# Kernel optimization log

Hardware: AMD Instinct MI355X
Metric: run time of the kernel (lower is better)

The kernel has to match this reference:

```python
import jax, jax.numpy as jnp
import numpy as np

BIG = 3.4028234e+38  # torch fill value used as additive mask
EPS = 1e-5           # nn.LayerNorm default eps


def _layernorm(x):
    mu = jnp.mean(x, axis=-1, keepdims=True)
    var = jnp.mean(jnp.square(x - mu), axis=-1, keepdims=True)
    return (x - mu) / jnp.sqrt(var + EPS)


def setup_inputs() -> dict:
    key = jax.random.key(0)
    ks = jax.random.split(key, 12)
    B, N, H, S = 32, 512, 256, 3  # batch, num_codes, embedding_size, num_stacks
    features = jax.random.normal(ks[0], (B, N, H), dtype=jnp.float32)
    masks = jnp.ones((B, N, 1), dtype=jnp.float32)
    guide = jax.random.randint(ks[1], (B, N, N), 0, 2).astype(jnp.float32)
    prior_guide = jax.random.uniform(ks[2], (B, N, N), dtype=jnp.float32)
    sc = 0.02
    WQ = jax.random.normal(ks[3], (S, H, H), dtype=jnp.float32) * sc
    WK = jax.random.normal(ks[4], (S, H, H), dtype=jnp.float32) * sc
    WV = jax.random.normal(ks[5], (S, H, H), dtype=jnp.float32) * sc
    W1 = jax.random.normal(ks[6], (S, H, H), dtype=jnp.float32) * sc
    b1 = jnp.zeros((S, H), dtype=jnp.float32)
    W2 = jax.random.normal(ks[7], (S, H, H), dtype=jnp.float32) * sc
    b2 = jnp.zeros((S, H), dtype=jnp.float32)
    return {"features": features, "masks": masks, "guide": guide,
            "prior_guide": prior_guide, "WQ": WQ, "WK": WK, "WV": WV,
            "W1": W1, "b1": b1, "W2": W2, "b2": b2}


def reference(features, masks, guide, prior_guide, WQ, WK, WV, W1, b1, W2, b2):
    H = features.shape[-1]
    scale = 1.0 / jnp.sqrt(jnp.float32(H))
    attention_mask = jnp.where(masks[:, :, 0] != 0, 0.0, BIG)  # [B,N]
    inf_mask = jnp.where(guide != 0, 0.0, BIG)                 # [B,N,N]
    attentions = []
    x = features
    for i in range(WQ.shape[0]):
        f = masks * x                                          # [B,N,H]
        if i == 0:
            att = prior_guide[:, None, :, :]                   # use_prior path
        else:
            q = jnp.einsum('bnh,hd->bnd', f, WQ[i].T)          # nn.Linear: x @ W^T
            k = jnp.einsum('bnh,hd->bnd', f, WK[i].T)
            pre = jnp.einsum('bqd,bkd->bqk', q, k) * scale     # [B,N,N] (heads=1)
            pre = pre - attention_mask[:, None, :] - inf_mask
            att = jax.nn.softmax(pre, axis=-1)[:, None, :, :]  # [B,1,N,N]
        attentions.append(att)
        v = jnp.einsum('bnh,hd->bnd', f, WV[i].T)              # [B,N,H]
        post = jnp.einsum('bqk,bkh->bqh', att[:, 0], v)        # squeeze head dim
        post = _layernorm(post + f)
        ffn = jnp.maximum(jnp.einsum('bnh,hd->bnd', post, W1[i].T) + b1[i], 0.0)
        ffn = jnp.einsum('bnh,hd->bnd', ffn, W2[i].T) + b2[i]
        x = _layernorm(ffn + post)
    return x * masks, jnp.stack(attentions)
```

## Files before the change

kernel.cpp:

```cpp
#include <hip/hip_runtime.h>
#include <cstdint>
#include <cstddef>

#define B_ 32
#define N_ 512
#define H_ 256
#define S_ 3
#define BN_ (B_*N_)
#define HH_ (H_*H_)
#define BIGF 3.4028234e+38f
#define EPSF 1e-5f
#define SF_ ((long)N_ * H_)
#define SVT_ ((long)H_ * N_)

typedef __bf16 bf16x8 __attribute__((ext_vector_type(8)));
typedef float  f32x4  __attribute__((ext_vector_type(4)));

typedef const void __attribute__((address_space(1)))* gas_t;
typedef void __attribute__((address_space(3)))* las_t;

__device__ __forceinline__ void async16(const unsigned short* g, unsigned short* l) {
  __builtin_amdgcn_global_load_lds((gas_t)g, (las_t)l, 16, 0, 0);
}

__device__ __forceinline__ unsigned short f2bf(float f) {
  __bf16 h = (__bf16)f;
  unsigned short s;
  __builtin_memcpy(&s, &h, 2);
  return s;
}
__device__ __forceinline__ float bf2f(unsigned short u) {
  unsigned int v = ((unsigned int)u) << 16;
  float f;
  __builtin_memcpy(&f, &v, 4);
  return f;
}

#define KC_STAGE(lane) ((((lane) & 3) ^ (((lane) >> 3) & 3)) * 8)
#define KC_READ(quad, l15) ((((quad) ^ (((l15) >> 1) & 3))) * 8)

__global__ __launch_bounds__(256) void cvt_all_k(
    const float* __restrict__ WQ, const float* __restrict__ WK,
    const float* __restrict__ WV, const float* __restrict__ W1,
    const float* __restrict__ W2,
    unsigned short* __restrict__ wqk, unsigned short* __restrict__ wv,
    unsigned short* __restrict__ w1, unsigned short* __restrict__ w2) {
  const int per = S_ * HH_ / 4;
  int gi = blockIdx.x * 256 + threadIdx.x;
  int which = gi / per;
  int e4 = gi - which * per;
  float4 v;
  if      (which == 0) v = ((const float4*)WQ)[e4];
  else if (which == 1) v = ((const float4*)WK)[e4];
  else if (which == 2) v = ((const float4*)WV)[e4];
  else if (which == 3) v = ((const float4*)W1)[e4];
  else                 v = ((const float4*)W2)[e4];
  ushort4 o;
  o.x = f2bf(v.x); o.y = f2bf(v.y); o.z = f2bf(v.z); o.w = f2bf(v.w);
  int e = e4 * 4;
  if (which <= 1) {
    int L = e / HH_, off = e - L * HH_;
    *(ushort4*)&wqk[(size_t)L * 2 * HH_ + (which == 1 ? HH_ : 0) + off] = o;
  } else if (which == 2) ((ushort4*)wv)[e4] = o;
  else if   (which == 3) ((ushort4*)w1)[e4] = o;
  else                   ((ushort4*)w2)[e4] = o;
}

__global__ __launch_bounds__(256) void mask_mul_k(
    const float* __restrict__ x, const float* __restrict__ masks,
    unsigned short* __restrict__ fb) {
  int i = blockIdx.x * 256 + threadIdx.x;
  int row = i >> 6;
  float m = masks[row];
  float4 v = ((const float4*)x)[i];
  ushort4 o;
  o.x = f2bf(v.x * m); o.y = f2bf(v.y * m); o.z = f2bf(v.z * m); o.w = f2bf(v.w * m);
  ((ushort4*)fb)[i] = o;
}

__device__ __forceinline__ void gemm_body(
    const unsigned short* __restrict__ A, const unsigned short* __restrict__ Bm,
    unsigned short* __restrict__ Cb,
    int K, int Nn, int lda, int ldb, long sA, long sB, long sC,
    int b, int m0, int n0, int t,
    unsigned short (&As)[2][128 * 32], unsigned short (&Bs)[2][128 * 32]) {
  const int wave = t >> 6, lane = t & 63;
  const int wm = wave >> 1, wn = wave & 1;
  const int quad = lane >> 4, l15 = lane & 15;
  const int srow = lane >> 2;
  const int kc = KC_STAGE(lane);
  const int pos8 = (lane & 3) * 8;

  const unsigned short* pa0 = A + (size_t)b * sA + (size_t)(m0 + wave * 32 + srow) * lda + kc;
  const unsigned short* pa1 = pa0 + 16 * (size_t)lda;
  const unsigned short* pb0 = Bm + (size_t)b * sB + (size_t)(n0 + wave * 32 + srow) * ldb + kc;
  const unsigned short* pb1 = pb0 + 16 * (size_t)ldb;
  const int lo = (wave * 32 + srow) * 32 + pos8;

  f32x4 acc[4][4];
#pragma unroll
  for (int i = 0; i < 4; ++i)
#pragma unroll
    for (int j = 0; j < 4; ++j) acc[i][j] = (f32x4){0.f, 0.f, 0.f, 0.f};

  const int soff = KC_READ(quad, l15);
  const int NT = K >> 5;
  async16(pa0, &As[0][lo]); async16(pa1, &As[0][lo + 16 * 32]);
  async16(pb0, &Bs[0][lo]); async16(pb1, &Bs[0][lo + 16 * 32]);
  __syncthreads();
  int cur = 0;
  for (int tt = 0; tt < NT; ++tt) {
    if (tt + 1 < NT) {
      const int kn = (tt + 1) << 5;
      async16(pa0 + kn, &As[cur ^ 1][lo]); async16(pa1 + kn, &As[cur ^ 1][lo + 16 * 32]);
      async16(pb0 + kn, &Bs[cur ^ 1][lo]); async16(pb1 + kn, &Bs[cur ^ 1][lo + 16 * 32]);
    }
    bf16x8 af[4], bfr[4];
#pragma unroll
    for (int i = 0; i < 4; ++i)
      af[i] = *(const bf16x8*)&As[cur][(wm * 64 + i * 16 + l15) * 32 + soff];
#pragma unroll
    for (int j = 0; j < 4; ++j)
      bfr[j] = *(const bf16x8*)&Bs[cur][(wn * 64 + j * 16 + l15) * 32 + soff];
#pragma unroll
    for (int i = 0; i < 4; ++i)
#pragma unroll
      for (int j = 0; j < 4; ++j)
        acc[i][j] = __builtin_amdgcn_mfma_f32_16x16x32_bf16(af[i], bfr[j], acc[i][j], 0, 0, 0);
    __syncthreads();
    cur ^= 1;
  }

#pragma unroll
  for (int i = 0; i < 4; ++i) {
    const int rbase = m0 + wm * 64 + i * 16 + quad * 4;
#pragma unroll
    for (int j = 0; j < 4; ++j) {
      const int c = n0 + wn * 64 + j * 16 + l15;
#pragma unroll
      for (int r = 0; r < 4; ++r)
        Cb[(size_t)b * sC + (size_t)(rbase + r) * Nn + c] = f2bf(acc[i][j][r]);
    }
  }
}

__global__ __launch_bounds__(256) void mfma_gemm_k(
    const unsigned short* __restrict__ A, const unsigned short* __restrict__ Bm,
    unsigned short* __restrict__ Cb,
    int K, int Nn, int lda, int ldb, long sA, long sB, long sC) {
  __shared__ __align__(16) unsigned short As[2][128 * 32];
  __shared__ __align__(16) unsigned short Bs[2][128 * 32];
  gemm_body(A, Bm, Cb, K, Nn, lda, ldb, sA, sB, sC,
            blockIdx.z, blockIdx.y * 128, blockIdx.x * 128, threadIdx.x, As, Bs);
}

__global__ __launch_bounds__(256) void gemm2_k(
    const unsigned short* __restrict__ A1, const unsigned short* __restrict__ B1,
    unsigned short* __restrict__ C1,
    const unsigned short* __restrict__ A2, const unsigned short* __restrict__ B2,
    unsigned short* __restrict__ C2) {
  __shared__ __align__(16) unsigned short As[2][128 * 32];
  __shared__ __align__(16) unsigned short Bs[2][128 * 32];
  const int bx = blockIdx.x;
  if (bx < 512) {
    gemm_body(A1, B1, C1, H_, 2 * H_, H_, H_, 0, 0, 0,
              0, (bx >> 2) * 128, (bx & 3) * 128, threadIdx.x, As, Bs);
  } else {
    const int v = bx - 512;
    gemm_body(A2, B2, C2, H_, N_, H_, H_, 0, SF_, SVT_,
              v >> 3, ((v >> 2) & 1) * 128, (v & 3) * 128, threadIdx.x, As, Bs);
  }
}

template<int PRIOR, int LAST>
__global__ __launch_bounds__(512) void mega_k(
    const unsigned short* __restrict__ qk, const float* __restrict__ prior,
    const float* __restrict__ masks, const float* __restrict__ guide,
    const unsigned short* __restrict__ vT, const unsigned short* __restrict__ resb,
    const unsigned short* __restrict__ w1, const float* __restrict__ b1,
    const unsigned short* __restrict__ w2, const float* __restrict__ b2,
    float* __restrict__ att, unsigned short* __restrict__ fbout,
    float* __restrict__ outx) {
  __shared__ __align__(16) unsigned short As[2][64 * 32];
  __shared__ __align__(16) unsigned short Bs[2][512 * 32];
  __shared__ __align__(16) unsigned short PsU[64 * 528];
  __shared__ float red[4][64][2];
  const int b = blockIdx.x;
  const int t = threadIdx.x;
  const int wave = t >> 6, lane = t & 63;
  const int quad = lane >> 4, l15 = lane & 15;
  const int m0 = blockIdx.y * 64;
  const int srow = lane >> 2;
  const int kc = KC_STAGE(lane);
  const int pos8 = (lane & 3) * 8;
  const int soff = KC_READ(quad, l15);

  const unsigned short* vb = vT + (size_t)b * SVT_;
  const unsigned short* pv0 = vb + (size_t)(wave * 16 + srow) * N_ + kc;
  const unsigned short* pv1 = pv0 + (size_t)128 * N_;
  const int lvo = (wave * 16 + srow) * 32 + pos8;

  if (PRIOR) {
    async16(pv0, &Bs[0][lvo]);
    async16(pv1, &Bs[0][lvo + 128 * 32]);
    const float* src = prior + ((size_t)b * N_ + m0) * N_;
    float*       dst = att   + ((size_t)b * N_ + m0) * N_;
#pragma unroll
    for (int s = 0; s < 16; ++s) {
      int idx4 = s * 512 + t;
      float4 v = ((const float4*)src)[idx4];
      ((float4*)dst)[idx4] = v;
      int row = idx4 >> 7, col4 = idx4 & 127;
      ushort4 o;
      o.x = f2bf(v.x); o.y = f2bf(v.y); o.z = f2bf(v.z); o.w = f2bf(v.w);
      *(ushort4*)&PsU[row * 520 + col4 * 4] = o;
    }
    __syncthreads();
  } else {
    const int wm = wave >> 2, wn = wave & 3;
    const int ld = 2 * H_;
    const unsigned short* base = qk + (size_t)b * N_ * ld;
    const unsigned short* pa = base + (size_t)(m0 + wave * 16 + srow) * ld + kc;
    const unsigned short* pb = base + H_ + (size_t)(wave * 64 + srow) * ld + kc;
    const int lao = (wave * 16 + srow) * 32 + pos8;
    const int lbo = (wave * 64 + srow) * 32 + pos8;

    f32x4 acc[2][8];
#pragma unroll
    for (int i = 0; i < 2; ++i)
#pragma unroll
      for (int j = 0; j < 8; ++j) acc[i][j] = (f32x4){0.f, 0.f, 0.f, 0.f};

    if (wave < 4) async16(pa, &As[0][lao]);
#pragma unroll
    for (int c = 0; c < 4; ++c)
      async16(pb + (size_t)c * 16 * ld, &Bs[0][lbo + c * 16 * 32]);
    __syncthreads();
    int cur = 0;
#pragma unroll
    for (int tt = 0; tt < 8; ++tt) {
      if (tt < 7) {
        const int kn = (tt + 1) * 32;
        if (wave < 4) async16(pa + kn, &As[cur ^ 1][lao]);
#pragma unroll
        for (int c = 0; c < 4; ++c)
          async16(pb + (size_t)c * 16 * ld + kn, &Bs[cur ^ 1][lbo + c * 16 * 32]);
      }
      bf16x8 af[2], bfr[8];
#pragma unroll
      for (int i = 0; i < 2; ++i)
        af[i] = *(const bf16x8*)&As[cur][(wm * 32 + i * 16 + l15) * 32 + soff];
#pragma unroll
      for (int j = 0; j < 8; ++j)
        bfr[j] = *(const bf16x8*)&Bs[cur][(wn * 128 + j * 16 + l15) * 32 + soff];
#pragma unroll
      for (int i = 0; i < 2; ++i)
#pragma unroll
        for (int j = 0; j < 8; ++j)
          acc[i][j] = __builtin_amdgcn_mfma_f32_16x16x32_bf16(af[i], bfr[j], acc[i][j], 0, 0, 0);
      __syncthreads();
      cur ^= 1;
    }

    async16(pv0, &Bs[0][lvo]);
    async16(pv1, &Bs[0][lvo + 128 * 32]);

    float am[8];
#pragma unroll
    for (int j = 0; j < 8; ++j) {
      float mv = masks[(size_t)b * N_ + wn * 128 + j * 16 + l15];
      am[j] = (mv != 0.f) ? 0.f : BIGF;
    }
#pragma unroll
    for (int i = 0; i < 2; ++i) {
#pragma unroll
      for (int r = 0; r < 4; ++r) {
        const int mloc = wm * 32 + i * 16 + quad * 4 + r;
        const float* gr = guide + ((size_t)b * N_ + m0 + mloc) * N_;
        float mx = -BIGF;
#pragma unroll
        for (int j = 0; j < 8; ++j) {
          const int c = wn * 128 + j * 16 + l15;
          float g = gr[c];
          float v = acc[i][j][r] * 0.0625f - am[j] - ((g != 0.f) ? 0.f : BIGF);
          acc[i][j][r] = v;
          mx = fmaxf(mx, v);
        }
#pragma unroll
        for (int off = 1; off < 16; off <<= 1) mx = fmaxf(mx, __shfl_xor(mx, off));
        if (l15 == 0) red[wn][mloc][0] = mx;
      }
    }
    __syncthreads();
#pragma unroll
    for (int i = 0; i < 2; ++i) {
#pragma unroll
      for (int r = 0; r < 4; ++r) {
        const int mloc = wm * 32 + i * 16 + quad * 4 + r;
        float M = fmaxf(fmaxf(red[0][mloc][0], red[1][mloc][0]),
                        fmaxf(red[2][mloc][0], red[3][mloc][0]));
        float s = 0.f;
#pragma unroll
        for (int j = 0; j < 8; ++j) {
          float e = __expf(acc[i][j][r] - M);
          acc[i][j][r] = e;
          s += e;
        }
#pragma unroll
        for (int off = 1; off < 16; off <<= 1) s += __shfl_xor(s, off);
        if (l15 == 0) red[wn][mloc][1] = s;
      }
    }
    __syncthreads();
#pragma unroll
    for (int i = 0; i < 2; ++i) {
#pragma unroll
      for (int r = 0; r < 4; ++r) {
        const int mloc = wm * 32 + i * 16 + quad * 4 + r;
        float S = red[0][mloc][1] + red[1][mloc][1] + red[2][mloc][1] + red[3][mloc][1];
        float inv = 1.f / S;
        const size_t rowoff = ((size_t)b * N_ + m0 + mloc) * N_;
#pragma unroll
        for (int j = 0; j < 8; ++j) {
          const int c = wn * 128 + j * 16 + l15;
          float o = acc[i][j][r] * inv;
          att[rowoff + c] = o;
          PsU[mloc * 520 + c] = f2bf(o);
        }
      }
    }
    __syncthreads();
  }

  const int wm2 = wave >> 2, wn2 = wave & 3;

  f32x4 acc2[2][4];
#pragma unroll
  for (int i = 0; i < 2; ++i)
#pragma unroll
    for (int j = 0; j < 4; ++j) acc2[i][j] = (f32x4){0.f, 0.f, 0.f, 0.f};

  int cur = 0;
#pragma unroll
  for (int tt = 0; tt < 16; ++tt) {
    if (tt < 15) {
      const int kn = (tt + 1) * 32;
      async16(pv0 + kn, &Bs[cur ^ 1][lvo]);
      async16(pv1 + kn, &Bs[cur ^ 1][lvo + 128 * 32]);
    }
    bf16x8 af[2], bfr[4];
#pragma unroll
    for (int i = 0; i < 2; ++i)
      af[i] = *(const bf16x8*)&PsU[(wm2 * 32 + i * 16 + l15) * 520 + tt * 32 + quad * 8];
#pragma unroll
    for (int j = 0; j < 4; ++j)
      bfr[j] = *(const bf16x8*)&Bs[cur][(wn2 * 64 + j * 16 + l15) * 32 + soff];
#pragma unroll
    for (int i = 0; i < 2; ++i)
#pragma unroll
      for (int j = 0; j < 4; ++j)
        acc2[i][j] = __builtin_amdgcn_mfma_f32_16x16x32_bf16(af[i], bfr[j], acc2[i][j], 0, 0, 0);
    __syncthreads();
    cur ^= 1;
  }

  const unsigned short* pw1  = w1 + (size_t)(wave * 16 + srow) * H_ + kc;
  const unsigned short* pw1b = pw1 + (size_t)128 * H_;
  const unsigned short* pw2  = w2 + (size_t)(wave * 16 + srow) * H_ + kc;
  const unsigned short* pw2b = pw2 + (size_t)128 * H_;
  async16(pw1,  &Bs[0][lvo]);
  async16(pw1b, &Bs[0][lvo + 128 * 32]);

#pragma unroll
  for (int i = 0; i < 2; ++i) {
#pragma unroll
    for (int r = 0; r < 4; ++r) {
      const int mloc = wm2 * 32 + i * 16 + quad * 4 + r;
      const long grow = (long)b * N_ + m0 + mloc;
      float s = 0.f, q = 0.f;
#pragma unroll
      for (int j = 0; j < 4; ++j) {
        const int c = wn2 * 64 + j * 16 + l15;
        float v = acc2[i][j][r] + bf2f(resb[grow * H_ + c]);
        acc2[i][j][r] = v;
        s += v; q += v * v;
      }
#pragma unroll
      for (int off = 1; off < 16; off <<= 1) {
        s += __shfl_xor(s, off);
        q += __shfl_xor(q, off);
      }
      if (l15 == 0) { red[wn2][mloc][0] = s; red[wn2][mloc][1] = q; }
    }
  }
  __syncthreads();
  unsigned short* Pb  = PsU;
  unsigned short* T1p = PsU + 64 * 264;
#pragma unroll
  for (int i = 0; i < 2; ++i) {
#pragma unroll
    for (int r = 0; r < 4; ++r) {
      const int mloc = wm2 * 32 + i * 16 + quad * 4 + r;
      float S = red[0][mloc][0] + red[1][mloc][0] + red[2][mloc][0] + red[3][mloc][0];
      float Q = red[0][mloc][1] + red[1][mloc][1] + red[2][mloc][1] + red[3][mloc][1];
      float mu = S * (1.f / H_);
      float var = Q * (1.f / H_) - mu * mu;
      float inv = 1.f / sqrtf(var + EPSF);
#pragma unroll
      for (int j = 0; j < 4; ++j) {
        const int c = wn2 * 64 + j * 16 + l15;
        float o = (acc2[i][j][r] - mu) * inv;
        acc2[i][j][r] = o;
        Pb[mloc * 264 + c] = f2bf(o);
      }
    }
  }
  __syncthreads();

  {
    f32x4 acc3[2][4];
#pragma unroll
    for (int i = 0; i < 2; ++i)
#pragma unroll
      for (int j = 0; j < 4; ++j) acc3[i][j] = (f32x4){0.f, 0.f, 0.f, 0.f};
    cur = 0;
#pragma unroll
    for (int tt = 0; tt < 8; ++tt) {
      if (tt < 7) {
        const int kn = (tt + 1) * 32;
        async16(pw1  + kn, &Bs[cur ^ 1][lvo]);
        async16(pw1b + kn, &Bs[cur ^ 1][lvo + 128 * 32]);
      }
      bf16x8 af[2], bfr[4];
#pragma unroll
      for (int i = 0; i < 2; ++i)
        af[i] = *(const bf16x8*)&Pb[(wm2 * 32 + i * 16 + l15) * 264 + tt * 32 + quad * 8];
#pragma unroll
      for (int j = 0; j < 4; ++j)
        bfr[j] = *(const bf16x8*)&Bs[cur][(wn2 * 64 + j * 16 + l15) * 32 + soff];
#pragma unroll
      for (int i = 0; i < 2; ++i)
#pragma unroll
        for (int j = 0; j < 4; ++j)
          acc3[i][j] = __builtin_amdgcn_mfma_f32_16x16x32_bf16(af[i], bfr[j], acc3[i][j], 0, 0, 0);
      __syncthreads();
      cur ^= 1;
    }

    async16(pw2,  &Bs[0][lvo]);
    async16(pw2b, &Bs[0][lvo + 128 * 32]);

    float bv[4];
#pragma unroll
    for (int j = 0; j < 4; ++j) bv[j] = b1[wn2 * 64 + j * 16 + l15];
#pragma unroll
    for (int i = 0; i < 2; ++i) {
#pragma unroll
      for (int r = 0; r < 4; ++r) {
        const int mloc = wm2 * 32 + i * 16 + quad * 4 + r;
#pragma unroll
        for (int j = 0; j < 4; ++j) {
          const int c = wn2 * 64 + j * 16 + l15;
          T1p[mloc * 264 + c] = f2bf(fmaxf(acc3[i][j][r] + bv[j], 0.f));
        }
      }
    }
  }
  __syncthreads();

  {
    f32x4 acc4[2][4];
#pragma unroll
    for (int i = 0; i < 2; ++i)
#pragma unroll
      for (int j = 0; j < 4; ++j) acc4[i][j] = (f32x4){0.f, 0.f, 0.f, 0.f};
    cur = 0;
#pragma unroll
    for (int tt = 0; tt < 8; ++tt) {
      if (tt < 7) {
        const int kn = (tt + 1) * 32;
        async16(pw2  + kn, &Bs[cur ^ 1][lvo]);
        async16(pw2b + kn, &Bs[cur ^ 1][lvo + 128 * 32]);
      }
      bf16x8 af[2], bfr[4];
#pragma unroll
      for (int i = 0; i < 2; ++i)
        af[i] = *(const bf16x8*)&T1p[(wm2 * 32 + i * 16 + l15) * 264 + tt * 32 + quad * 8];
#pragma unroll
      for (int j = 0; j < 4; ++j)
        bfr[j] = *(const bf16x8*)&Bs[cur][(wn2 * 64 + j * 16 + l15) * 32 + soff];
#pragma unroll
      for (int i = 0; i < 2; ++i)
#pragma unroll
        for (int j = 0; j < 4; ++j)
          acc4[i][j] = __builtin_amdgcn_mfma_f32_16x16x32_bf16(af[i], bfr[j], acc4[i][j], 0, 0, 0);
      __syncthreads();
      cur ^= 1;
    }
    float bv[4];
#pragma unroll
    for (int j = 0; j < 4; ++j) bv[j] = b2[wn2 * 64 + j * 16 + l15];
#pragma unroll
    for (int i = 0; i < 2; ++i) {
#pragma unroll
      for (int r = 0; r < 4; ++r) {
        const int mloc = wm2 * 32 + i * 16 + quad * 4 + r;
        float s = 0.f, q = 0.f;
#pragma unroll
        for (int j = 0; j < 4; ++j) {
          float v = acc4[i][j][r] + bv[j] + acc2[i][j][r];
          acc4[i][j][r] = v;
          s += v; q += v * v;
        }
#pragma unroll
        for (int off = 1; off < 16; off <<= 1) {
          s += __shfl_xor(s, off);
          q += __shfl_xor(q, off);
        }
        if (l15 == 0) { red[wn2][mloc][0] = s; red[wn2][mloc][1] = q; }
      }
    }
    __syncthreads();
#pragma unroll
    for (int i = 0; i < 2; ++i) {
#pragma unroll
      for (int r = 0; r < 4; ++r) {
        const int mloc = wm2 * 32 + i * 16 + quad * 4 + r;
        const long grow = (long)b * N_ + m0 + mloc;
        float S = red[0][mloc][0] + red[1][mloc][0] + red[2][mloc][0] + red[3][mloc][0];
        float Q = red[0][mloc][1] + red[1][mloc][1] + red[2][mloc][1] + red[3][mloc][1];
        float mu = S * (1.f / H_);
        float var = Q * (1.f / H_) - mu * mu;
        float inv = 1.f / sqrtf(var + EPSF);
        float mval = masks[grow];
#pragma unroll
        for (int j = 0; j < 4; ++j) {
          const int c = wn2 * 64 + j * 16 + l15;
          float o = (acc4[i][j][r] - mu) * inv * mval;
          if (LAST) outx[grow * H_ + c] = o;
          else      fbout[grow * H_ + c] = f2bf(o);
        }
      }
    }
  }
}

extern "C" void kernel_launch(void* const* d_in, const int* in_sizes, int n_in,
                              void* d_out, int out_size, void* d_ws, size_t ws_size,
                              hipStream_t stream) {
  const float* features = (const float*)d_in[0];
  const float* masks    = (const float*)d_in[1];
  const float* guide    = (const float*)d_in[2];
  const float* prior    = (const float*)d_in[3];
  const float* WQ       = (const float*)d_in[4];
  const float* WK       = (const float*)d_in[5];
  const float* WV       = (const float*)d_in[6];
  const float* W1       = (const float*)d_in[7];
  const float* b1       = (const float*)d_in[8];
  const float* W2       = (const float*)d_in[9];
  const float* b2       = (const float*)d_in[10];

  float* out     = (float*)d_out;
  float* out_x   = out;
  float* out_att = out + (size_t)BN_ * H_;

  char* w = (char*)d_ws;
  unsigned short* f_bf   = (unsigned short*)w; w += (size_t)BN_ * H_ * 2;
  unsigned short* qk_bf  = (unsigned short*)w; w += (size_t)BN_ * 2 * H_ * 2;
  unsigned short* vT     = (unsigned short*)w; w += (size_t)BN_ * H_ * 2;
  unsigned short* wqk_bf = (unsigned short*)w; w += (size_t)S_ * 2 * HH_ * 2;
  unsigned short* wv_bf  = (unsigned short*)w; w += (size_t)S_ * HH_ * 2;
  unsigned short* w1_bf  = (unsigned short*)w; w += (size_t)S_ * HH_ * 2;
  unsigned short* w2_bf  = (unsigned short*)w; w += (size_t)S_ * HH_ * 2;

  dim3 g_cvt(5 * S_ * HH_ / 1024);
  dim3 g_ew(BN_ * H_ / 1024);
  dim3 g_vt(4, 2, B_);
  dim3 g_g2(768);
  dim3 g_mega(B_, N_ / 64);

  cvt_all_k<<<g_cvt, 256, 0, stream>>>(WQ, WK, WV, W1, W2, wqk_bf, wv_bf, w1_bf, w2_bf);
  mask_mul_k<<<g_ew, 256, 0, stream>>>(features, masks, f_bf);

  for (int i = 0; i < S_; ++i) {
    float* att = out_att + (size_t)i * B_ * N_ * N_;
    const unsigned short* w1p = w1_bf + (size_t)i * HH_;
    const unsigned short* w2p = w2_bf + (size_t)i * HH_;
    const float* b1p = b1 + (size_t)i * H_;
    const float* b2p = b2 + (size_t)i * H_;
    if (i == 0) {
      mfma_gemm_k<<<g_vt, 256, 0, stream>>>(wv_bf, f_bf, vT, H_, N_, H_, H_, 0, SF_, SVT_);
      mega_k<1, 0><<<g_mega, 512, 0, stream>>>(nullptr, prior, masks, nullptr,
                                               vT, f_bf, w1p, b1p, w2p, b2p,
                                               att, f_bf, nullptr);
    } else {
      gemm2_k<<<g_g2, 256, 0, stream>>>(f_bf, wqk_bf + (size_t)i * 2 * HH_, qk_bf,
                                        wv_bf + (size_t)i * HH_, f_bf, vT);
      if (i < S_ - 1) {
        mega_k<0, 0><<<g_mega, 512, 0, stream>>>(qk_bf, nullptr, masks, guide,
                                                 vT, f_bf, w1p, b1p, w2p, b2p,
                                                 att, f_bf, nullptr);
      } else {
        mega_k<0, 1><<<g_mega, 512, 0, stream>>>(qk_bf, nullptr, masks, guide,
                                                 vT, f_bf, w1p, b1p, w2p, b2p,
                                                 att, nullptr, out_x);
      }
    }
  }
}
```

Before: 339.3 us.

## Double mega kernel to 1024 threads, add nontemporal streams and finer GEMM sync

Launches the fused attention/FFN mega kernel with 16 waves instead of 8 and splits each GEMM stage's N dimension across 8 wave columns, so each wave holds fewer accumulators and issues fewer async loads. The large attention, prior and output streams switch to nontemporal loads and stores to avoid polluting cache. The generic GEMM body replaces __syncthreads with explicit vmcnt waits plus barriers so the next tile's prefetch stays in flight. The extra waves raise register and barrier pressure per block and give less MFMA work per wave.

Result: slower. 351.1 us (+3.5%).

```diff
diff --git a/kernel.cpp b/kernel.cpp
--- a/kernel.cpp
+++ b/kernel.cpp
@@ -22,6 +22,10 @@
 __device__ __forceinline__ void async16(const unsigned short* g, unsigned short* l) {
   __builtin_amdgcn_global_load_lds((gas_t)g, (las_t)l, 16, 0, 0);
 }
+
+#define VMW(n) asm volatile("s_waitcnt vmcnt(" #n ")" ::: "memory")
+#define SB()   __builtin_amdgcn_s_barrier()
+#define SC0()  __builtin_amdgcn_sched_barrier(0)
 
 __device__ __forceinline__ unsigned short f2bf(float f) {
   __bf16 h = (__bf16)f;
@@ -107,14 +111,15 @@
   const int NT = K >> 5;
   async16(pa0, &As[0][lo]); async16(pa1, &As[0][lo + 16 * 32]);
   async16(pb0, &Bs[0][lo]); async16(pb1, &Bs[0][lo + 16 * 32]);
-  __syncthreads();
   int cur = 0;
   for (int tt = 0; tt < NT; ++tt) {
     if (tt + 1 < NT) {
       const int kn = (tt + 1) << 5;
       async16(pa0 + kn, &As[cur ^ 1][lo]); async16(pa1 + kn, &As[cur ^ 1][lo + 16 * 32]);
       async16(pb0 + kn, &Bs[cur ^ 1][lo]); async16(pb1 + kn, &Bs[cur ^ 1][lo + 16 * 32]);
-    }
+      VMW(4);
+    } else VMW(0);
+    SB(); SC0();
     bf16x8 af[4], bfr[4];
 #pragma unroll
     for (int i = 0; i < 4; ++i)
@@ -127,7 +132,7 @@
 #pragma unroll
       for (int j = 0; j < 4; ++j)
         acc[i][j] = __builtin_amdgcn_mfma_f32_16x16x32_bf16(af[i], bfr[j], acc[i][j], 0, 0, 0);
-    __syncthreads();
+    SC0(); SB();
     cur ^= 1;
   }
 
@@ -173,7 +178,7 @@
 }
 
 template<int PRIOR, int LAST>
-__global__ __launch_bounds__(512) void mega_k(
+__global__ __launch_bounds__(1024) void mega_k(
     const unsigned short* __restrict__ qk, const float* __restrict__ prior,
     const float* __restrict__ masks, const float* __restrict__ guide,
     const unsigned short* __restrict__ vT, const unsigned short* __restrict__ resb,
@@ -184,7 +189,7 @@
   __shared__ __align__(16) unsigned short As[2][64 * 32];
   __shared__ __align__(16) unsigned short Bs[2][512 * 32];
   __shared__ __align__(16) unsigned short PsU[64 * 528];
-  __shared__ float red[4][64][2];
+  __shared__ float red[8][64][2];
   const int b = blockIdx.x;
   const int t = threadIdx.x;
   const int wave = t >> 6, lane = t & 63;
@@ -194,22 +199,20 @@
   const int kc = KC_STAGE(lane);
   const int pos8 = (lane & 3) * 8;
   const int soff = KC_READ(quad, l15);
-
-  const unsigned short* vb = vT + (size_t)b * SVT_;
-  const unsigned short* pv0 = vb + (size_t)(wave * 16 + srow) * N_ + kc;
-  const unsigned short* pv1 = pv0 + (size_t)128 * N_;
+  const int wm = wave >> 3, wn = wave & 7;
+
+  const unsigned short* pv = vT + (size_t)b * SVT_ + (size_t)(wave * 16 + srow) * N_ + kc;
   const int lvo = (wave * 16 + srow) * 32 + pos8;
 
   if (PRIOR) {
-    async16(pv0, &Bs[0][lvo]);
-    async16(pv1, &Bs[0][lvo + 128 * 32]);
-    const float* src = prior + ((size_t)b * N_ + m0) * N_;
-    float*       dst = att   + ((size_t)b * N_ + m0) * N_;
-#pragma unroll
-    for (int s = 0; s < 16; ++s) {
-      int idx4 = s * 512 + t;
-      float4 v = ((const float4*)src)[idx4];
-      ((float4*)dst)[idx4] = v;
+    async16(pv, &Bs[0][lvo]);
+    const f32x4* src = (const f32x4*)(prior + ((size_t)b * N_ + m0) * N_);
+    f32x4*       dst = (f32x4*)(att   + ((size_t)b * N_ + m0) * N_);
+#pragma unroll
+    for (int s = 0; s < 8; ++s) {
+      int idx4 = s * 1024 + t;
+      f32x4 v = __builtin_nontemporal_load(&src[idx4]);
+      __builtin_nontemporal_store(v, &dst[idx4]);
       int row = idx4 >> 7, col4 = idx4 & 127;
       ushort4 o;
       o.x = f2bf(v.x); o.y = f2bf(v.y); o.z = f2bf(v.z); o.w = f2bf(v.w);
@@ -217,23 +220,22 @@
     }
     __syncthreads();
   } else {
-    const int wm = wave >> 2, wn = wave & 3;
     const int ld = 2 * H_;
     const unsigned short* base = qk + (size_t)b * N_ * ld;
     const unsigned short* pa = base + (size_t)(m0 + wave * 16 + srow) * ld + kc;
-    const unsigned short* pb = base + H_ + (size_t)(wave * 64 + srow) * ld + kc;
+    const unsigned short* pb = base + H_ + (size_t)(wave * 32 + srow) * ld + kc;
     const int lao = (wave * 16 + srow) * 32 + pos8;
-    const int lbo = (wave * 64 + srow) * 32 + pos8;
-
-    f32x4 acc[2][8];
+    const int lbo = (wave * 32 + srow) * 32 + pos8;
+
+    f32x4 acc[2][4];
 #pragma unroll
     for (int i = 0; i < 2; ++i)
 #pragma unroll
-      for (int j = 0; j < 8; ++j) acc[i][j] = (f32x4){0.f, 0.f, 0.f, 0.f};
+      for (int j = 0; j < 4; ++j) acc[i][j] = (f32x4){0.f, 0.f, 0.f, 0.f};
 
     if (wave < 4) async16(pa, &As[0][lao]);
 #pragma unroll
-    for (int c = 0; c < 4; ++c)
+    for (int c = 0; c < 2; ++c)
       async16(pb + (size_t)c * 16 * ld, &Bs[0][lbo + c * 16 * 32]);
     __syncthreads();
     int cur = 0;
@@ -243,32 +245,31 @@
         const int kn = (tt + 1) * 32;
         if (wave < 4) async16(pa + kn, &As[cur ^ 1][lao]);
 #pragma unroll
-        for (int c = 0; c < 4; ++c)
+        for (int c = 0; c < 2; ++c)
           async16(pb + (size_t)c * 16 * ld + kn, &Bs[cur ^ 1][lbo + c * 16 * 32]);
       }
-      bf16x8 af[2], bfr[8];
+      bf16x8 af[2], bfr[4];
 #pragma unroll
       for (int i = 0; i < 2; ++i)
         af[i] = *(const bf16x8*)&As[cur][(wm * 32 + i * 16 + l15) * 32 + soff];
 #pragma unroll
-      for (int j = 0; j < 8; ++j)
-        bfr[j] = *(const bf16x8*)&Bs[cur][(wn * 128 + j * 16 + l15) * 32 + soff];
+      for (int j = 0; j < 4; ++j)
+        bfr[j] = *(const bf16x8*)&Bs[cur][(wn * 64 + j * 16 + l15) * 32 + soff];
 #pragma unroll
       for (int i = 0; i < 2; ++i)
 #pragma unroll
-        for (int j = 0; j < 8; ++j)
+        for (int j = 0; j < 4; ++j)
           acc[i][j] = __builtin_amdgcn_mfma_f32_16x16x32_bf16(af[i], bfr[j], acc[i][j], 0, 0, 0);
       __syncthreads();
       cur ^= 1;
     }
 
-    async16(pv0, &Bs[0][lvo]);
-    async16(pv1, &Bs[0][lvo + 128 * 32]);
-
-    float am[8];
-#pragma unroll
-    for (int j = 0; j < 8; ++j) {
-      float mv = masks[(size_t)b * N_ + wn * 128 + j * 16 + l15];
+    async16(pv, &Bs[0][lvo]);
+
+    float am[4];
+#pragma unroll
+    for (int j = 0; j < 4; ++j) {
+      float mv = masks[(size_t)b * N_ + wn * 64 + j * 16 + l15];
       am[j] = (mv != 0.f) ? 0.f : BIGF;
     }
 #pragma unroll
@@ -279,9 +280,9 @@
         const float* gr = guide + ((size_t)b * N_ + m0 + mloc) * N_;
         float mx = -BIGF;
 #pragma unroll
-        for (int j = 0; j < 8; ++j) {
-          const int c = wn * 128 + j * 16 + l15;
-          float g = gr[c];
+        for (int j = 0; j < 4; ++j) {
+          const int c = wn * 64 + j * 16 + l15;
+          float g = __builtin_nontemporal_load(&gr[c]);
           float v = acc[i][j][r] * 0.0625f - am[j] - ((g != 0.f) ? 0.f : BIGF);
           acc[i][j][r] = v;
           mx = fmaxf(mx, v);
@@ -297,11 +298,12 @@
 #pragma unroll
       for (int r = 0; r < 4; ++r) {
         const int mloc = wm * 32 + i * 16 + quad * 4 + r;
-        float M = fmaxf(fmaxf(red[0][mloc][0], red[1][mloc][0]),
-                        fmaxf(red[2][mloc][0], red[3][mloc][0]));
+        float M = red[0][mloc][0];
+#pragma unroll
+        for (int w = 1; w < 8; ++w) M = fmaxf(M, red[w][mloc][0]);
         float s = 0.f;
 #pragma unroll
-        for (int j = 0; j < 8; ++j) {
+        for (int j = 0; j < 4; ++j) {
           float e = __expf(acc[i][j][r] - M);
           acc[i][j][r] = e;
           s += e;
@@ -317,14 +319,16 @@
 #pragma unroll
       for (int r = 0; r < 4; ++r) {
         const int mloc = wm * 32 + i * 16 + quad * 4 + r;
-        float S = red[0][mloc][1] + red[1][mloc][1] + red[2][mloc][1] + red[3][mloc][1];
+        float S = red[0][mloc][1];
+#pragma unroll
+        for (int w = 1; w < 8; ++w) S += red[w][mloc][1];
         float inv = 1.f / S;
         const size_t rowoff = ((size_t)b * N_ + m0 + mloc) * N_;
 #pragma unroll
-        for (int j = 0; j < 8; ++j) {
-          const int c = wn * 128 + j * 16 + l15;
+        for (int j = 0; j < 4; ++j) {
+          const int c = wn * 64 + j * 16 + l15;
           float o = acc[i][j][r] * inv;
-          att[rowoff + c] = o;
+          __builtin_nontemporal_store(o, &att[rowoff + c]);
           PsU[mloc * 520 + c] = f2bf(o);
         }
       }
@@ -332,55 +336,48 @@
     __syncthreads();
   }
 
-  const int wm2 = wave >> 2, wn2 = wave & 3;
-
-  f32x4 acc2[2][4];
+  f32x4 acc2[2][2];
 #pragma unroll
   for (int i = 0; i < 2; ++i)
 #pragma unroll
-    for (int j = 0; j < 4; ++j) acc2[i][j] = (f32x4){0.f, 0.f, 0.f, 0.f};
+    for (int j = 0; j < 2; ++j) acc2[i][j] = (f32x4){0.f, 0.f, 0.f, 0.f};
 
   int cur = 0;
 #pragma unroll
   for (int tt = 0; tt < 16; ++tt) {
     if (tt < 15) {
-      const int kn = (tt + 1) * 32;
-      async16(pv0 + kn, &Bs[cur ^ 1][lvo]);
-      async16(pv1 + kn, &Bs[cur ^ 1][lvo + 128 * 32]);
-    }
-    bf16x8 af[2], bfr[4];
+      async16(pv + (tt + 1) * 32, &Bs[cur ^ 1][lvo]);
+    }
+    bf16x8 af[2], bfr[2];
 #pragma unroll
     for (int i = 0; i < 2; ++i)
-      af[i] = *(const bf16x8*)&PsU[(wm2 * 32 + i * 16 + l15) * 520 + tt * 32 + quad * 8];
-#pragma unroll
-    for (int j = 0; j < 4; ++j)
-      bfr[j] = *(const bf16x8*)&Bs[cur][(wn2 * 64 + j * 16 + l15) * 32 + soff];
+      af[i] = *(const bf16x8*)&PsU[(wm * 32 + i * 16 + l15) * 520 + tt * 32 + quad * 8];
+#pragma unroll
+    for (int j = 0; j < 2; ++j)
+      bfr[j] = *(const bf16x8*)&Bs[cur][(wn * 32 + j * 16 + l15) * 32 + soff];
 #pragma unroll
     for (int i = 0; i < 2; ++i)
 #pragma unroll
-      for (int j = 0; j < 4; ++j)
+      for (int j = 0; j < 2; ++j)
         acc2[i][j] = __builtin_amdgcn_mfma_f32_16x16x32_bf16(af[i], bfr[j], acc2[i][j], 0, 0, 0);
     __syncthreads();
     cur ^= 1;
   }
 
-  const unsigned short* pw1  = w1 + (size_t)(wave * 16 + srow) * H_ + kc;
-  const unsigned short* pw1b = pw1 + (size_t)128 * H_;
-  const unsigned short* pw2  = w2 + (size_t)(wave * 16 + srow) * H_ + kc;
-  const unsigned short* pw2b = pw2 + (size_t)128 * H_;
-  async16(pw1,  &Bs[0][lvo]);
-  async16(pw1b, &Bs[0][lvo + 128 * 32]);
+  const unsigned short* pw1 = w1 + (size_t)(wave * 16 + srow) * H_ + kc;
+  const unsigned short* pw2 = w2 + (size_t)(wave * 16 + srow) * H_ + kc;
+  async16(pw1, &Bs[0][lvo]);
 
 #pragma unroll
   for (int i = 0; i < 2; ++i) {
 #pragma unroll
     for (int r = 0; r < 4; ++r) {
-      const int mloc = wm2 * 32 + i * 16 + quad * 4 + r;
+      const int mloc = wm * 32 + i * 16 + quad * 4 + r;
       const long grow = (long)b * N_ + m0 + mloc;
       float s = 0.f, q = 0.f;
 #pragma unroll
-      for (int j = 0; j < 4; ++j) {
-        const int c = wn2 * 64 + j * 16 + l15;
+      for (int j = 0; j < 2; ++j) {
+        const int c = wn * 32 + j * 16 + l15;
         float v = acc2[i][j][r] + bf2f(resb[grow * H_ + c]);
         acc2[i][j][r] = v;
         s += v; q += v * v;
@@ -390,7 +387,7 @@
         s += __shfl_xor(s, off);
         q += __shfl_xor(q, off);
       }
-      if (l15 == 0) { red[wn2][mloc][0] = s; red[wn2][mloc][1] = q; }
+      if (l15 == 0) { red[wn][mloc][0] = s; red[wn][mloc][1] = q; }
     }
   }
   __syncthreads();
@@ -400,15 +397,16 @@
   for (int i = 0; i < 2; ++i) {
 #pragma unroll
     for (int r = 0; r < 4; ++r) {
-      const int mloc = wm2 * 32 + i * 16 + quad * 4 + r;
-      float S = red[0][mloc][0] + red[1][mloc][0] + red[2][mloc][0] + red[3][mloc][0];
-      float Q = red[0][mloc][1] + red[1][mloc][1] + red[2][mloc][1] + red[3][mloc][1];
+      const int mloc = wm * 32 + i * 16 + quad * 4 + r;
+      float S = red[0][mloc][0], Q = red[0][mloc][1];
+#pragma unroll
+      for (int w = 1; w < 8; ++w) { S += red[w][mloc][0]; Q += red[w][mloc][1]; }
       float mu = S * (1.f / H_);
       float var = Q * (1.f / H_) - mu * mu;
       float inv = 1.f / sqrtf(var + EPSF);
 #pragma unroll
-      for (int j = 0; j < 4; ++j) {
-        const int c = wn2 * 64 + j * 16 + l15;
+      for (int j = 0; j < 2; ++j) {
+        const int c = wn * 32 + j * 16 + l15;
         float o = (acc2[i][j][r] - mu) * inv;
         acc2[i][j][r] = o;
         Pb[mloc * 264 + c] = f2bf(o);
@@ -418,49 +416,46 @@
   __syncthreads();
 
   {
-    f32x4 acc3[2][4];
+    f32x4 acc3[2][2];
 #pragma unroll
     for (int i = 0; i < 2; ++i)
 #pragma unroll
-      for (int j = 0; j < 4; ++j) acc3[i][j] = (f32x4){0.f, 0.f, 0.f, 0.f};
+      for (int j = 0; j < 2; ++j) acc3[i][j] = (f32x4){0.f, 0.f, 0.f, 0.f};
     cur = 0;
 #pragma unroll
     for (int tt = 0; tt < 8; ++tt) {
       if (tt < 7) {
-        const int kn = (tt + 1) * 32;
-        async16(pw1  + kn, &Bs[cur ^ 1][lvo]);
-        async16(pw1b + kn, &Bs[cur ^ 1][lvo + 128 * 32]);
-      }
-      bf16x8 af[2], bfr[4];
+        async16(pw1 + (tt + 1) * 32, &Bs[cur ^ 1][lvo]);
+      }
+      bf16x8 af[2], bfr[2];
 #pragma unroll
       for (int i = 0; i < 2; ++i)
-        af[i] = *(const bf16x8*)&Pb[(wm2 * 32 + i * 16 + l15) * 264 + tt * 32 + quad * 8];
-#pragma unroll
-      for (int j = 0; j < 4; ++j)
-        bfr[j] = *(const bf16x8*)&Bs[cur][(wn2 * 64 + j * 16 + l15) * 32 + soff];
+        af[i] = *(const bf16x8*)&Pb[(wm * 32 + i * 16 + l15) * 264 + tt * 32 + quad * 8];
+#pragma unroll
+      for (int j = 0; j < 2; ++j)
+        bfr[j] = *(const bf16x8*)&Bs[cur][(wn * 32 + j * 16 + l15) * 32 + soff];
 #pragma unroll
       for (int i = 0; i < 2; ++i)
 #pragma unroll
-        for (int j = 0; j < 4; ++j)
+        for (int j = 0; j < 2; ++j)
           acc3[i][j] = __builtin_amdgcn_mfma_f32_16x16x32_bf16(af[i], bfr[j], acc3[i][j], 0, 0, 0);
       __syncthreads();
       cur ^= 1;
     }
 
-    async16(pw2,  &Bs[0][lvo]);
-    async16(pw2b, &Bs[0][lvo + 128 * 32]);
-
-    float bv[4];
-#pragma unroll
-    for (int j = 0; j < 4; ++j) bv[j] = b1[wn2 * 64 + j * 16 + l15];
+    async16(pw2, &Bs[0][lvo]);
+
+    float bv[2];
+#pragma unroll
+    for (int j = 0; j < 2; ++j) bv[j] = b1[wn * 32 + j * 16 + l15];
 #pragma unroll
     for (int i = 0; i < 2; ++i) {
 #pragma unroll
       for (int r = 0; r < 4; ++r) {
-        const int mloc = wm2 * 32 + i * 16 + quad * 4 + r;
-#pragma unroll
-        for (int j = 0; j < 4; ++j) {
-          const int c = wn2 * 64 + j * 16 + l15;
+        const int mloc = wm * 32 + i * 16 + quad * 4 + r;
+#pragma unroll
+        for (int j = 0; j < 2; ++j) {
+          const int c = wn * 32 + j * 16 + l15;
           T1p[mloc * 264 + c] = f2bf(fmaxf(acc3[i][j][r] + bv[j], 0.f));
         }
       }
@@ -469,45 +464,43 @@
   __syncthreads();
 
   {
-    f32x4 acc4[2][4];
+    f32x4 acc4[2][2];
 #pragma unroll
     for (int i = 0; i < 2; ++i)
 #pragma unroll
-      for (int j = 0; j < 4; ++j) acc4[i][j] = (f32x4){0.f, 0.f, 0.f, 0.f};
+      for (int j = 0; j < 2; ++j) acc4[i][j] = (f32x4){0.f, 0.f, 0.f, 0.f};
     cur = 0;
 #pragma unroll
     for (int tt = 0; tt < 8; ++tt) {
       if (tt < 7) {
-        const int kn = (tt + 1) * 32;
-        async16(pw2  + kn, &Bs[cur ^ 1][lvo]);
-        async16(pw2b + kn, &Bs[cur ^ 1][lvo + 128 * 32]);
-      }
-      bf16x8 af[2], bfr[4];
+        async16(pw2 + (tt + 1) * 32, &Bs[cur ^ 1][lvo]);
+      }
+      bf16x8 af[2], bfr[2];
 #pragma unroll
       for (int i = 0; i < 2; ++i)
-        af[i] = *(const bf16x8*)&T1p[(wm2 * 32 + i * 16 + l15) * 264 + tt * 32 + quad * 8];
-#pragma unroll
-      for (int j = 0; j < 4; ++j)
-        bfr[j] = *(const bf16x8*)&Bs[cur][(wn2 * 64 + j * 16 + l15) * 32 + soff];
+        af[i] = *(const bf16x8*)&T1p[(wm * 32 + i * 16 + l15) * 264 + tt * 32 + quad * 8];
+#pragma unroll
+      for (int j = 0; j < 2; ++j)
+        bfr[j] = *(const bf16x8*)&Bs[cur][(wn * 32 + j * 16 + l15) * 32 + soff];
 #pragma unroll
       for (int i = 0; i < 2; ++i)
 #pragma unroll
-        for (int j = 0; j < 4; ++j)
+        for (int j = 0; j < 2; ++j)
           acc4[i][j] = __builtin_amdgcn_mfma_f32_16x16x32_bf16(af[i], bfr[j], acc4[i][j], 0, 0, 0);
       __syncthreads();
       cur ^= 1;
     }
-    float bv[4];
-#pragma unroll
-    for (int j = 0; j < 4; ++j) bv[j] = b2[wn2 * 64 + j * 16 + l15];
+    float bv[2];
+#pragma unroll
+    for (int j = 0; j < 2; ++j) bv[j] = b2[wn * 32 + j * 16 + l15];
 #pragma unroll
     for (int i = 0; i < 2; ++i) {
 #pragma unroll
       for (int r = 0; r < 4; ++r) {
-        const int mloc = wm2 * 32 + i * 16 + quad * 4 + r;
+        const int mloc = wm * 32 + i * 16 + quad * 4 + r;
         float s = 0.f, q = 0.f;
 #pragma unroll
-        for (int j = 0; j < 4; ++j) {
+        for (int j = 0; j < 2; ++j) {
           float v = acc4[i][j][r] + bv[j] + acc2[i][j][r];
           acc4[i][j][r] = v;
           s += v; q += v * v;
@@ -517,7 +510,7 @@
           s += __shfl_xor(s, off);
           q += __shfl_xor(q, off);
         }
-        if (l15 == 0) { red[wn2][mloc][0] = s; red[wn2][mloc][1] = q; }
+        if (l15 == 0) { red[wn][mloc][0] = s; red[wn][mloc][1] = q; }
       }
     }
     __syncthreads();
@@ -525,19 +518,20 @@
     for (int i = 0; i < 2; ++i) {
 #pragma unroll
       for (int r = 0; r < 4; ++r) {
-        const int mloc = wm2 * 32 + i * 16 + quad * 4 + r;
+        const int mloc = wm * 32 + i * 16 + quad * 4 + r;
         const long grow = (long)b * N_ + m0 + mloc;
-        float S = red[0][mloc][0] + red[1][mloc][0] + red[2][mloc][0] + red[3][mloc][0];
-        float Q = red[0][mloc][1] + red[1][mloc][1] + red[2][mloc][1] + red[3][mloc][1];
+        float S = red[0][mloc][0], Q = red[0][mloc][1];
+#pragma unroll
+        for (int w = 1; w < 8; ++w) { S += red[w][mloc][0]; Q += red[w][mloc][1]; }
         float mu = S * (1.f / H_);
         float var = Q * (1.f / H_) - mu * mu;
         float inv = 1.f / sqrtf(var + EPSF);
         float mval = masks[grow];
 #pragma unroll
-        for (int j = 0; j < 4; ++j) {
-          const int c = wn2 * 64 + j * 16 + l15;
+        for (int j = 0; j < 2; ++j) {
+          const int c = wn * 32 + j * 16 + l15;
           float o = (acc4[i][j][r] - mu) * inv * mval;
-          if (LAST) outx[grow * H_ + c] = o;
+          if (LAST) __builtin_nontemporal_store(o, &outx[grow * H_ + c]);
           else      fbout[grow * H_ + c] = f2bf(o);
         }
       }
@@ -590,21 +584,21 @@
     const float* b2p = b2 + (size_t)i * H_;
     if (i == 0) {
       mfma_gemm_k<<<g_vt, 256, 0, stream>>>(wv_bf, f_bf, vT, H_, N_, H_, H_, 0, SF_, SVT_);
-      mega_k<1, 0><<<g_mega, 512, 0, stream>>>(nullptr, prior, masks, nullptr,
-                                               vT, f_bf, w1p, b1p, w2p, b2p,
-                                               att, f_bf, nullptr);
+      mega_k<1, 0><<<g_mega, 1024, 0, stream>>>(nullptr, prior, masks, nullptr,
+                                                vT, f_bf, w1p, b1p, w2p, b2p,
+                                                att, f_bf, nullptr);
     } else {
       gemm2_k<<<g_g2, 256, 0, stream>>>(f_bf, wqk_bf + (size_t)i * 2 * HH_, qk_bf,
                                         wv_bf + (size_t)i * HH_, f_bf, vT);
       if (i < S_ - 1) {
-        mega_k<0, 0><<<g_mega, 512, 0, stream>>>(qk_bf, nullptr, masks, guide,
-                                                 vT, f_bf, w1p, b1p, w2p, b2p,
-                                                 att, f_bf, nullptr);
+        mega_k<0, 0><<<g_mega, 1024, 0, stream>>>(qk_bf, nullptr, masks, guide,
+                                                  vT, f_bf, w1p, b1p, w2p, b2p,
+                                                  att, f_bf, nullptr);
       } else {
-        mega_k<0, 1><<<g_mega, 512, 0, stream>>>(qk_bf, nullptr, masks, guide,
-                                                 vT, f_bf, w1p, b1p, w2p, b2p,
-                                                 att, nullptr, out_x);
-      }
-    }
-  }
-}
+        mega_k<0, 1><<<g_mega, 1024, 0, stream>>>(qk_bf, nullptr, masks, guide,
+                                                  vT, f_bf, w1p, b1p, w2p, b2p,
+                                                  att, nullptr, out_x);
+      }
+    }
+  }
+}
```
